# Kernel tuning notes

Hardware: AMD Instinct MI355X
Metric: run time of the kernel (lower is better)

Reference implementation:

```python
import math
import jax, jax.numpy as jnp
import numpy as np

F, B, J, D, H = 120, 64, 22, 512, 4  # frames, batch, joints, d_model, heads
DFF = 2048
EPS = 1e-6


def setup_inputs() -> dict:
    key = jax.random.key(0)
    ks = jax.random.split(key, 32)
    w = lambda k, s: jax.random.normal(k, s, jnp.float32) * 0.02
    inp = {
        "x": jax.random.normal(ks[0], (F, B, J, D), jnp.float32),
        "timesteps_embs": jax.random.normal(ks[1], (1, B, D), jnp.float32),
        "spat_mask": jnp.ones((1, 1, 1, 1, 1), jnp.int32),
        "temp_mask": jnp.ones((1, 1, 1, 1, 1), jnp.int32),
        "layer_ind": 1,
    }
    i = 2
    for p in ("s", "t"):  # spatial / temporal attention params
        for m in ("q", "k", "v", "o"):
            inp[p + "W" + m] = w(ks[i], (D, D)); i += 1
            inp[p + "b" + m] = w(ks[i], (D,)); i += 1
    inp["ffW1"] = w(ks[i], (D, DFF)); inp["ffb1"] = w(ks[i + 1], (DFF,))
    inp["ffW2"] = w(ks[i + 2], (DFF, D)); inp["ffb2"] = w(ks[i + 3], (D,))
    for n in ("n1", "n2", "n3"):
        inp[n + "a"] = jnp.ones((D,), jnp.float32)
        inp[n + "b"] = jnp.zeros((D,), jnp.float32)
    return inp


def _norm(x, a, b):
    # custom Norm: uses torch.std (ddof=1) and eps added to std (not var)
    mu = jnp.mean(x, axis=-1, keepdims=True)
    sd = jnp.std(x, axis=-1, ddof=1, keepdims=True)
    return a * (x - mu) / (sd + EPS) + b


def _mha(x, Wq, bq, Wk, bk, Wv, bv, Wo, bo, h, mask):
    d1, bs, d2, dm = x.shape
    dk = dm // h
    split = lambda t: (t.reshape(d1, bs, d2, h, dk)).transpose(0, 1, 3, 2, 4)  # (d1,bs,h,d2,dk)
    q = split(x @ Wq + bq)
    k = split(x @ Wk + bk)
    v = split(x @ Wv + bv)
    scores = jnp.einsum("fbhqd,fbhkd->fbhqk", q, k) / math.sqrt(dk)
    m = jnp.swapaxes(mask, 0, 1).astype(jnp.float32)  # mask.transpose(0,1).float()
    scores = jnp.where(m == 0, -1e9, scores)
    p = jax.nn.softmax(scores, axis=-1)
    o = jnp.einsum("fbhqk,fbhkd->fbhqd", p, v)
    o = o.transpose(0, 1, 3, 2, 4).reshape(d1, bs, d2, dm)
    return o @ Wo + bo


def _forward(x, timesteps_embs,
             sWq, sbq, sWk, sbk, sWv, sbv, sWo, sbo,
             tWq, tbq, tWk, tbk, tWv, tbv, tWo, tbo,
             ffW1, ffb1, ffW2, ffb2,
             n1a, n1b, n2a, n2b, n3a, n3b,
             spat_mask, temp_mask):
    # layer_ind > 0 path: no positional-encoding additions (eval mode: dropout = identity)
    f, bs, nj, dm = x.shape
    ts = jnp.broadcast_to(timesteps_embs[:, :, None, :], (f, bs, 1, dm))
    x1 = jnp.concatenate([ts, x], axis=2)                      # (F,B,J+1,D)
    x1 = x + _mha(x1, sWq, sbq, sWk, sbk, sWv, sbv, sWo, sbo, H, spat_mask)[:, :, 1:, :]
    x1 = jnp.swapaxes(_norm(x1, n1a, n1b), 0, 2)               # (J,B,F,D)
    ts2 = jnp.broadcast_to(timesteps_embs[:, :, None, :], (x1.shape[0], bs, 1, dm))
    x2 = jnp.concatenate([ts2, x1], axis=2)                    # (J,B,F+1,D)
    x2 = x1 + _mha(x2, tWq, tbq, tWk, tbk, tWv, tbv, tWo, tbo, H, temp_mask)[:, :, 1:, :]
    x2 = jnp.swapaxes(_norm(x2, n2a, n2b), 0, 2)               # (F,B,J,D)
    ff = jax.nn.gelu(x2 @ ffW1 + ffb1, approximate=False) @ ffW2 + ffb2
    return _norm(x2 + ff, n3a, n3b)


def reference(x, timesteps_embs,
              sWq, sbq, sWk, sbk, sWv, sbv, sWo, sbo,
              tWq, tbq, tWk, tbk, tWv, tbv, tWo, tbo,
              ffW1, ffb1, ffW2, ffb2,
              n1a, n1b, n2a, n2b, n3a, n3b,
              spat_mask, temp_mask, layer_ind):
    # layer_ind is fixed to 1 (layer_ind==0 branch is unreachable/broken in source)
    return _forward(x, timesteps_embs,
                    sWq, sbq, sWk, sbk, sWv, sbv, sWo, sbo,
                    tWq, tbq, tWk, tbk, tWv, tbv, tWo, tbo,
                    ffW1, ffb1, ffW2, ffb2,
                    n1a, n1b, n2a, n2b, n3a, n3b,
                    spat_mask, temp_mask)
```

## Files before the change

kernel.cpp:

```cpp
#include <hip/hip_runtime.h>
#include <hip/hip_bf16.h>
#include <math.h>


#define F_DIM 120
#define B_DIM 64
#define J_DIM 22
#define H_DIM 4
#define M_TOK (F_DIM * B_DIM * J_DIM)

#define DEV static __device__ __forceinline__

typedef short bf16x8 __attribute__((ext_vector_type(8)));
typedef short us8 __attribute__((ext_vector_type(8)));
typedef float f32x4 __attribute__((ext_vector_type(4)));

struct __align__(8) us4 { unsigned short x, y, z, w; };

DEV unsigned short f2b(float f) {
  unsigned u = __float_as_uint(f);
  u += 0x7fffu + ((u >> 16) & 1u);
  return (unsigned short)(u >> 16);
}
DEV float b2f(unsigned short u) { return __uint_as_float(((unsigned)u) << 16); }

#define GLOAD16(g, l)                                                          \
  __builtin_amdgcn_global_load_lds(                                            \
      (const __attribute__((address_space(1))) void*)(g),                      \
      (__attribute__((address_space(3))) void*)(l), 16, 0, 0)

enum { EPI_QKV = 0, EPI_GELU = 1, EPI_RES = 2, EPI_ACC = 3, EPI_RESB = 4,
       EPI_ROB = 5,
       EPI_RBB = 6 };

__global__ __launch_bounds__(256)
void cast_k(const float* __restrict__ in, unsigned short* __restrict__ out, int n8) {
  for (int i = blockIdx.x * 256 + threadIdx.x; i < n8; i += gridDim.x * 256) {
    const float4 a = ((const float4*)in)[i * 2];
    const float4 b = ((const float4*)in)[i * 2 + 1];
    us8 v;
    v[0] = f2b(a.x); v[1] = f2b(a.y); v[2] = f2b(a.z); v[3] = f2b(a.w);
    v[4] = f2b(b.x); v[5] = f2b(b.y); v[6] = f2b(b.z); v[7] = f2b(b.w);
    *(us8*)&out[i * 8] = v;
  }
}

__global__ __launch_bounds__(256)
void tcast_k(const float* __restrict__ W, unsigned short* __restrict__ WT, int K, int N) {
  __shared__ float t[32][33];
  const int n0 = blockIdx.x * 32, k0 = blockIdx.y * 32;
  const int tx = threadIdx.x, ty = threadIdx.y;
#pragma unroll
  for (int i = 0; i < 4; ++i)
    t[ty + i * 8][tx] = W[(size_t)(k0 + ty + i * 8) * N + n0 + tx];
  __syncthreads();
#pragma unroll
  for (int i = 0; i < 4; ++i)
    WT[(size_t)(n0 + ty + i * 8) * K + k0 + tx] = f2b(t[tx][ty + i * 8]);
}

struct Tc8Args { const float* W[8]; unsigned short* WT[8]; };
__global__ __launch_bounds__(256)
void tcast8_k(Tc8Args a) {
  __shared__ float t[32][33];
  const float* W = a.W[blockIdx.z];
  unsigned short* WT = a.WT[blockIdx.z];
  const int n0 = blockIdx.x * 32, k0 = blockIdx.y * 32;
  const int tx = threadIdx.x, ty = threadIdx.y;
#pragma unroll
  for (int i = 0; i < 4; ++i)
    t[ty + i * 8][tx] = W[(size_t)(k0 + ty + i * 8) * 512 + n0 + tx];
  __syncthreads();
#pragma unroll
  for (int i = 0; i < 4; ++i)
    WT[(size_t)(n0 + ty + i * 8) * 512 + k0 + tx] = f2b(t[tx][ty + i * 8]);
}

struct TsArgs { const float* W[4]; const float* bias[4]; unsigned short* out[4]; };
__global__ __launch_bounds__(1024)
void tsproj_k(const float* __restrict__ ts, TsArgs a) {
  __shared__ float tsr[512];
  __shared__ float red[3][256];
  const int b = blockIdx.x;
  const int nb = blockIdx.y;
  const int pj = blockIdx.z;
  const int t = threadIdx.x;
  const int n = nb * 256 + (t & 255);
  const int kh = t >> 8;
  if (t < 512) tsr[t] = ts[b * 512 + t];
  __syncthreads();
  const float* W = a.W[pj];
  float acc = 0.f;
  const int k0 = kh * 128;
  for (int k = k0; k < k0 + 128; ++k)
    acc += tsr[k] * W[(size_t)k * 512 + n];
  if (kh) red[kh - 1][t & 255] = acc;
  __syncthreads();
  if (kh == 0) {
    acc += red[0][t & 255] + red[1][t & 255] + red[2][t & 255];
    a.out[pj][b * 512 + n] = f2b(acc + a.bias[pj][n]);
  }
}

template<int EPI>
DEV void epi_store(float v, int row, int col, const float* b0, const float* b1,
                   const float* b2, const void* res, float* outF,
                   unsigned short* o0, unsigned short* o1, unsigned short* o2,
                   int ldo, float scale) {
  if constexpr (EPI == EPI_QKV) {
    const int seg = col >> 9;
    const int cl = col & 511;
    const float* bs = (seg == 0) ? b0 : (seg == 1) ? b1 : b2;
    unsigned short* ob = (seg == 0) ? o0 : (seg == 1) ? o1 : o2;
    const float sc = (seg == 0) ? scale : 1.f;
    v = (v + bs[cl]) * sc;
    ob[(size_t)row * 512 + cl] = f2b(v);
  } else if constexpr (EPI == EPI_GELU) {
    v += b0[col];
    const float a2 = 1.5957691216057308f * (v + 0.044715f * v * v * v);
    const float g = v / (1.f + __expf(-a2));
    o0[(size_t)row * ldo + col] = f2b(g);
  } else if constexpr (EPI == EPI_RES) {
    const size_t off = (size_t)row * 512 + col;
    outF[off] = v + b0[col] + ((const float*)res)[off];
  } else if constexpr (EPI == EPI_RESB) {
    const size_t off = (size_t)row * 512 + col;
    outF[off] = v + b0[col] + b2f(((const unsigned short*)res)[off]);
  } else if constexpr (EPI == EPI_ROB) {
    const size_t off = (size_t)row * 512 + col;
    o0[off] = f2b(v + b0[col] + ((const float*)res)[off]);
  } else if constexpr (EPI == EPI_RBB) {
    const size_t off = (size_t)row * 512 + col;
    o0[off] = f2b(v + b0[col] + b2f(((const unsigned short*)res)[off]));
  } else {
    const size_t off = (size_t)row * 512 + col;
    outF[off] = v + outF[off];
  }
}

template<int EPI>
__global__ __launch_bounds__(512, 4)
void gemm256_k(const unsigned short* __restrict__ Ab, const unsigned short* __restrict__ Wt,
               const float* __restrict__ b0, const float* __restrict__ b1, const float* __restrict__ b2,
               const void* __restrict__ res, float* __restrict__ outF,
               unsigned short* __restrict__ o0, unsigned short* __restrict__ o1, unsigned short* __restrict__ o2,
               int lda, int ldw, int ldo, int nk, int nx, float scale) {
  __shared__ unsigned short As[3][8192];
  __shared__ unsigned short Bs[3][4096];
  const int tid = threadIdx.x;
  const int chunkg = gridDim.x >> 3;
  const int wg = (blockIdx.x & 7) * chunkg + (blockIdx.x >> 3);
  const int nbase = (wg % nx) * 128;
  const int mbase = (wg / nx) * 256;
  const int lane = tid & 63;
  const int w = tid >> 6;
  const int wr = (w >> 1) * 64;
  const int wc = (w & 1) * 64;
  const int l15 = lane & 15;
  const int lhi = lane >> 4;

  const int crow = lane >> 2;
  const int ccol = (((lane & 3) ^ ((lane >> 3) & 3)) << 3);
  const unsigned short* gA0 = Ab + (size_t)(mbase + 32 * w + crow) * lda + ccol;
  const unsigned short* gA1 = gA0 + (size_t)16 * lda;
  const unsigned short* gB0 = Wt + (size_t)(nbase + 16 * w + crow) * ldw + ccol;

  auto stage = [&](int bb, int kt) {
    GLOAD16(gA0 + kt, &As[bb][(2 * w) * 512]);
    GLOAD16(gA1 + kt, &As[bb][(2 * w + 1) * 512]);
    GLOAD16(gB0 + kt, &Bs[bb][w * 512]);
  };

  f32x4 acc[4][4] = {};
  const int KT = nk >> 5;
  const int swz = ((lhi ^ ((l15 >> 1) & 3)) << 3);

  stage(0, 0);
  stage(1, 32);
  asm volatile("s_waitcnt vmcnt(3)" ::: "memory");
  __builtin_amdgcn_s_barrier();

  for (int t = 0; t < KT; ++t) {
    const unsigned short* as = As[t % 3];
    const unsigned short* bs = Bs[t % 3];
    if (t + 2 < KT) stage((t + 2) % 3, (t + 2) << 5);
    bf16x8 afr[4], bfr[4];
#pragma unroll
    for (int i = 0; i < 4; ++i) afr[i] = *(const bf16x8*)&as[(wr + i * 16 + l15) * 32 + swz];
#pragma unroll
    for (int j = 0; j < 4; ++j) bfr[j] = *(const bf16x8*)&bs[(wc + j * 16 + l15) * 32 + swz];
#pragma unroll
    for (int i = 0; i < 4; ++i)
#pragma unroll
      for (int j = 0; j < 4; ++j)
        acc[i][j] = __builtin_amdgcn_mfma_f32_16x16x32_bf16(afr[i], bfr[j], acc[i][j], 0, 0, 0);
    if (t + 2 < KT)      asm volatile("s_waitcnt vmcnt(3) lgkmcnt(0)" ::: "memory");
    else if (t + 1 < KT) asm volatile("s_waitcnt vmcnt(0) lgkmcnt(0)" ::: "memory");
    else                 asm volatile("s_waitcnt lgkmcnt(0)" ::: "memory");
    __builtin_amdgcn_s_barrier();
  }

#pragma unroll
  for (int i = 0; i < 4; ++i)
#pragma unroll
    for (int j = 0; j < 4; ++j) {
      const int row0 = mbase + wr + i * 16 + (lhi << 2);
      const int col = nbase + wc + j * 16 + l15;
#pragma unroll
      for (int q = 0; q < 4; ++q)
        epi_store<EPI>(acc[i][j][q], row0 + q, col, b0, b1, b2, res, outF, o0, o1, o2, ldo, scale);
    }
}

template<int EPI>
__global__ __launch_bounds__(256)
void gemm_k(const unsigned short* __restrict__ Ab, const unsigned short* __restrict__ Wt,
            const float* __restrict__ b0, const float* __restrict__ b1, const float* __restrict__ b2,
            const void* __restrict__ res, float* __restrict__ outF,
            unsigned short* __restrict__ o0, unsigned short* __restrict__ o1, unsigned short* __restrict__ o2,
            int lda, int ldw, int ldo, int nk, int nx, float scale) {
  __shared__ unsigned short As[3][4096];
  __shared__ unsigned short Bs[3][4096];
  const int tid = threadIdx.x;
  const int chunkg = gridDim.x >> 3;
  const int wg = (blockIdx.x & 7) * chunkg + (blockIdx.x >> 3);
  const int nbase = (wg % nx) * 128;
  const int mbase = (wg / nx) * 128;
  const int lane = tid & 63;
  const int w = tid >> 6;
  const int wr = (w >> 1) * 64;
  const int wc = (w & 1) * 64;
  const int l15 = lane & 15;
  const int lhi = lane >> 4;

  const int crow = lane >> 2;
  const int ccol = (((lane & 3) ^ ((lane >> 3) & 3)) << 3);
  const unsigned short* gA0 = Ab + (size_t)(mbase + 32 * w + crow) * lda + ccol;
  const unsigned short* gA1 = gA0 + (size_t)16 * lda;
  const unsigned short* gB0 = Wt + (size_t)(nbase + 32 * w + crow) * ldw + ccol;
  const unsigned short* gB1 = gB0 + (size_t)16 * ldw;

  auto stage = [&](int bb, int kt) {
    GLOAD16(gA0 + kt, &As[bb][(2 * w) * 512]);
    GLOAD16(gA1 + kt, &As[bb][(2 * w + 1) * 512]);
    GLOAD16(gB0 + kt, &Bs[bb][(2 * w) * 512]);
    GLOAD16(gB1 + kt, &Bs[bb][(2 * w + 1) * 512]);
  };

  f32x4 acc[4][4] = {};
  const int KT = nk >> 5;
  const int swz = ((lhi ^ ((l15 >> 1) & 3)) << 3);

  stage(0, 0);
  stage(1, 32);
  asm volatile("s_waitcnt vmcnt(4)" ::: "memory");
  __builtin_amdgcn_s_barrier();

  for (int t = 0; t < KT; ++t) {
    const unsigned short* as = As[t % 3];
    const unsigned short* bs = Bs[t % 3];
    if (t + 2 < KT) stage((t + 2) % 3, (t + 2) << 5);
    bf16x8 afr[4], bfr[4];
#pragma unroll
    for (int i = 0; i < 4; ++i) afr[i] = *(const bf16x8*)&as[(wr + i * 16 + l15) * 32 + swz];
#pragma unroll
    for (int j = 0; j < 4; ++j) bfr[j] = *(const bf16x8*)&bs[(wc + j * 16 + l15) * 32 + swz];
#pragma unroll
    for (int i = 0; i < 4; ++i)
#pragma unroll
      for (int j = 0; j < 4; ++j)
        acc[i][j] = __builtin_amdgcn_mfma_f32_16x16x32_bf16(afr[i], bfr[j], acc[i][j], 0, 0, 0);
    if (t + 2 < KT)      asm volatile("s_waitcnt vmcnt(4) lgkmcnt(0)" ::: "memory");
    else if (t + 1 < KT) asm volatile("s_waitcnt vmcnt(0) lgkmcnt(0)" ::: "memory");
    else                 asm volatile("s_waitcnt lgkmcnt(0)" ::: "memory");
    __builtin_amdgcn_s_barrier();
  }

#pragma unroll
  for (int i = 0; i < 4; ++i)
#pragma unroll
    for (int j = 0; j < 4; ++j) {
      const int row0 = mbase + wr + i * 16 + (lhi << 2);
      const int col = nbase + wc + j * 16 + l15;
#pragma unroll
      for (int q = 0; q < 4; ++q)
        epi_store<EPI>(acc[i][j][q], row0 + q, col, b0, b1, b2, res, outF, o0, o1, o2, ldo, scale);
    }
}

template<int EPI>
__global__ __launch_bounds__(256)
void gemmf_k(const float* __restrict__ Af, const unsigned short* __restrict__ Wt,
             const float* __restrict__ b0, const float* __restrict__ b1, const float* __restrict__ b2,
             const void* __restrict__ res, float* __restrict__ outF,
             unsigned short* __restrict__ o0, unsigned short* __restrict__ o1, unsigned short* __restrict__ o2,
             int lda, int ldw, int ldo, int nk, int nx, float scale) {
  __shared__ unsigned short As[128][40];
  __shared__ unsigned short Bs[128][40];
  const int tid = threadIdx.x;
  const int chunkg = gridDim.x >> 3;
  const int wg = (blockIdx.x & 7) * chunkg + (blockIdx.x >> 3);
  const int nbase = (wg % nx) * 128;
  const int mbase = (wg / nx) * 128;
  const int lane = tid & 63;
  const int w = tid >> 6;
  const int wr = (w >> 1) * 64;
  const int wc = (w & 1) * 64;
  const int l15 = lane & 15;
  const int lhi = lane >> 4;

  float4 ra[4];
  us4 rb[4];
  auto loadAB = [&](int kt) {
#pragma unroll
    for (int i = 0; i < 4; ++i) {
      const int g = i * 256 + tid;
      const int r = g >> 3;
      const int c = (g & 7) << 2;
      ra[i] = *(const float4*)(Af + (size_t)(mbase + r) * lda + kt + c);
      rb[i] = *(const us4*)(Wt + (size_t)(nbase + r) * ldw + kt + c);
    }
  };
  auto storeAB = [&]() {
#pragma unroll
    for (int i = 0; i < 4; ++i) {
      const int g = i * 256 + tid;
      const int r = g >> 3;
      const int c = (g & 7) << 2;
      us4 ua;
      ua.x = f2b(ra[i].x); ua.y = f2b(ra[i].y); ua.z = f2b(ra[i].z); ua.w = f2b(ra[i].w);
      *(us4*)&As[r][c] = ua;
      *(us4*)&Bs[r][c] = rb[i];
    }
  };

  f32x4 acc[4][4] = {};
  const int KT = nk >> 5;
  loadAB(0);
  storeAB();
  __syncthreads();
  for (int t = 0; t < KT; ++t) {
    if (t + 1 < KT) loadAB((t + 1) << 5);
    bf16x8 afr[4], bfr[4];
    const int klo = lhi << 3;
#pragma unroll
    for (int i = 0; i < 4; ++i) afr[i] = *(const bf16x8*)&As[wr + i * 16 + l15][klo];
#pragma unroll
    for (int j = 0; j < 4; ++j) bfr[j] = *(const bf16x8*)&Bs[wc + j * 16 + l15][klo];
#pragma unroll
    for (int i = 0; i < 4; ++i)
#pragma unroll
      for (int j = 0; j < 4; ++j)
        acc[i][j] = __builtin_amdgcn_mfma_f32_16x16x32_bf16(afr[i], bfr[j], acc[i][j], 0, 0, 0);
    __syncthreads();
    if (t + 1 < KT) { storeAB(); __syncthreads(); }
  }

#pragma unroll
  for (int i = 0; i < 4; ++i)
#pragma unroll
    for (int j = 0; j < 4; ++j) {
      const int row0 = mbase + wr + i * 16 + (lhi << 2);
      const int col = nbase + wc + j * 16 + l15;
#pragma unroll
      for (int q = 0; q < 4; ++q)
        epi_store<EPI>(acc[i][j][q], row0 + q, col, b0, b1, b2, res, outF, o0, o1, o2, ldo, scale);
    }
}

__global__ __launch_bounds__(256)
void attn_t_k(const unsigned short* __restrict__ Qb, const unsigned short* __restrict__ Kb,
              const unsigned short* __restrict__ Vb, const unsigned short* __restrict__ kts,
              const unsigned short* __restrict__ vts, unsigned short* __restrict__ Ob) {
  __shared__ unsigned short Ps[128][134];
  __shared__ unsigned short Vt[64][134];
  const int tid = threadIdx.x;
  const int inst = blockIdx.x >> 2;
  const int h = blockIdx.x & 3;
  const int b = inst & (B_DIM - 1);
  const size_t rowbase = (size_t)inst * 120;
  const int hoff = h * 128;
  const int lane = tid & 63;
  const int w = tid >> 6;
  const int wr = w * 32;
  const int l15 = lane & 15;
  const int lhi = lane >> 4;

  auto stageV = [&](int half) {
    for (int e = tid; e < 2048; e += 256) {
      const int d4 = (e & 15) << 2;
      const int key = e >> 4;
      us4 v;
      if (key <= 120) {
        const unsigned short* src = (key == 0) ? (vts + b * 512) : (Vb + (rowbase + key - 1) * 512);
        v = *(const us4*)(src + hoff + half * 64 + d4);
      } else { v.x = 0; v.y = 0; v.z = 0; v.w = 0; }
      Vt[d4 + 0][key] = v.x; Vt[d4 + 1][key] = v.y; Vt[d4 + 2][key] = v.z; Vt[d4 + 3][key] = v.w;
    }
  };
  stageV(0);

  bf16x8 qa[2][4];
#pragma unroll
  for (int i = 0; i < 2; ++i) {
    const int row = min(wr + i * 16 + l15, 119);
    const unsigned short* qp = Qb + (rowbase + row) * 512 + hoff;
#pragma unroll
    for (int kt = 0; kt < 4; ++kt)
      qa[i][kt] = *(const bf16x8*)(qp + kt * 32 + lhi * 8);
  }

  f32x4 acc[2][8] = {};
#pragma unroll
  for (int kt = 0; kt < 4; ++kt) {
    const int klo = kt * 32 + lhi * 8;
    bf16x8 kb[8];
#pragma unroll
    for (int j = 0; j < 8; ++j) {
      const int key = min(j * 16 + l15, 120);
      const unsigned short* kp = (key == 0) ? (kts + b * 512) : (Kb + (rowbase + key - 1) * 512);
      kb[j] = *(const bf16x8*)(kp + hoff + klo);
    }
#pragma unroll
    for (int i = 0; i < 2; ++i)
#pragma unroll
      for (int j = 0; j < 8; ++j)
        acc[i][j] = __builtin_amdgcn_mfma_f32_16x16x32_bf16(qa[i][kt], kb[j], acc[i][j], 0, 0, 0);
  }

  float rinv[2][4];
#pragma unroll
  for (int i = 0; i < 2; ++i)
#pragma unroll
    for (int q = 0; q < 4; ++q) {
      float m = -1e30f;
#pragma unroll
      for (int j = 0; j < 8; ++j)
        if (j * 16 + l15 <= 120) m = fmaxf(m, acc[i][j][q]);
#pragma unroll
      for (int mk = 1; mk < 16; mk <<= 1) m = fmaxf(m, __shfl_xor(m, mk, 64));
      float s = 0.f;
#pragma unroll
      for (int j = 0; j < 8; ++j) {
        const float e = (j * 16 + l15 <= 120) ? __expf(acc[i][j][q] - m) : 0.f;
        acc[i][j][q] = e; s += e;
      }
#pragma unroll
      for (int mk = 1; mk < 16; mk <<= 1) s += __shfl_xor(s, mk, 64);
      rinv[i][q] = 1.f / s;
    }

#pragma unroll
  for (int i = 0; i < 2; ++i)
#pragma unroll
    for (int j = 0; j < 8; ++j)
#pragma unroll
      for (int q = 0; q < 4; ++q)
        Ps[wr + i * 16 + lhi * 4 + q][j * 16 + l15] = f2b(acc[i][j][q]);

  __syncthreads();

#pragma unroll
  for (int half = 0; half < 2; ++half) {
    if (half == 1) {
      __syncthreads();
      stageV(1);
      __syncthreads();
    }
    f32x4 oac[2][4] = {};
#pragma unroll
    for (int kt = 0; kt < 4; ++kt) {
      const int klo = kt * 32 + lhi * 8;
      bf16x8 pa[2], vb[4];
#pragma unroll
      for (int i = 0; i < 2; ++i) pa[i] = *(const bf16x8*)&Ps[wr + i * 16 + l15][klo];
#pragma unroll
      for (int jd = 0; jd < 4; ++jd) vb[jd] = *(const bf16x8*)&Vt[jd * 16 + l15][klo];
#pragma unroll
      for (int i = 0; i < 2; ++i)
#pragma unroll
        for (int jd = 0; jd < 4; ++jd)
          oac[i][jd] = __builtin_amdgcn_mfma_f32_16x16x32_bf16(pa[i], vb[jd], oac[i][jd], 0, 0, 0);
    }
#pragma unroll
    for (int i = 0; i < 2; ++i)
#pragma unroll
      for (int q = 0; q < 4; ++q) {
        const int r = wr + i * 16 + lhi * 4 + q;
        if (r < 120) {
          const float sc = rinv[i][q];
#pragma unroll
          for (int jd = 0; jd < 4; ++jd)
            Ob[(rowbase + r) * 512 + hoff + half * 64 + jd * 16 + l15] = f2b(oac[i][jd][q] * sc);
        }
      }
  }
}

__global__ __launch_bounds__(256)
void attn_s_k(const unsigned short* __restrict__ Qb, const unsigned short* __restrict__ Kb,
              const unsigned short* __restrict__ Vb, const unsigned short* __restrict__ kts,
              const unsigned short* __restrict__ vts, unsigned short* __restrict__ Ob) {
  __shared__ unsigned short Ps[4][32][34];
  __shared__ unsigned short Vt[4][128][34];
  const int tid = threadIdx.x;
  const int inst = blockIdx.x;
  const int b = inst & (B_DIM - 1);
  const size_t rowbase = (size_t)inst * 22;
  const int lane = tid & 63;
  const int h = tid >> 6;
  const int l15 = lane & 15;
  const int lhi = lane >> 4;
  const int hoff = h * 128;

  for (int e = tid; e < 4096; e += 256) {
    const int h2 = e >> 10;
    const int rem = e & 1023;
    const int key = rem >> 5;
    const int d4 = (rem & 31) << 2;
    us4 v;
    if (key <= 22) {
      const unsigned short* src = (key == 0) ? (vts + b * 512) : (Vb + (rowbase + key - 1) * 512);
      v = *(const us4*)(src + h2 * 128 + d4);
    } else { v.x = 0; v.y = 0; v.z = 0; v.w = 0; }
    Vt[h2][d4 + 0][key] = v.x; Vt[h2][d4 + 1][key] = v.y; Vt[h2][d4 + 2][key] = v.z; Vt[h2][d4 + 3][key] = v.w;
  }

  bf16x8 qa[2][4];
#pragma unroll
  for (int i = 0; i < 2; ++i) {
    const int row = min(i * 16 + l15, 21);
    const unsigned short* qp = Qb + (rowbase + row) * 512 + hoff;
#pragma unroll
    for (int kt = 0; kt < 4; ++kt)
      qa[i][kt] = *(const bf16x8*)(qp + kt * 32 + lhi * 8);
  }

  f32x4 acc[2][2] = {};
#pragma unroll
  for (int kt = 0; kt < 4; ++kt) {
    const int klo = kt * 32 + lhi * 8;
    bf16x8 kb[2];
#pragma unroll
    for (int j = 0; j < 2; ++j) {
      const int key = min(j * 16 + l15, 22);
      const unsigned short* kp = (key == 0) ? (kts + b * 512) : (Kb + (rowbase + key - 1) * 512);
      kb[j] = *(const bf16x8*)(kp + hoff + klo);
    }
#pragma unroll
    for (int i = 0; i < 2; ++i)
#pragma unroll
      for (int j = 0; j < 2; ++j)
        acc[i][j] = __builtin_amdgcn_mfma_f32_16x16x32_bf16(qa[i][kt], kb[j], acc[i][j], 0, 0, 0);
  }

  float rinv[2][4];
#pragma unroll
  for (int i = 0; i < 2; ++i)
#pragma unroll
    for (int q = 0; q < 4; ++q) {
      float m = -1e30f;
#pragma unroll
      for (int j = 0; j < 2; ++j)
        if (j * 16 + l15 <= 22) m = fmaxf(m, acc[i][j][q]);
#pragma unroll
      for (int mk = 1; mk < 16; mk <<= 1) m = fmaxf(m, __shfl_xor(m, mk, 64));
      float s = 0.f;
#pragma unroll
      for (int j = 0; j < 2; ++j) {
        const float e = (j * 16 + l15 <= 22) ? __expf(acc[i][j][q] - m) : 0.f;
        acc[i][j][q] = e; s += e;
      }
#pragma unroll
      for (int mk = 1; mk < 16; mk <<= 1) s += __shfl_xor(s, mk, 64);
      rinv[i][q] = 1.f / s;
    }

#pragma unroll
  for (int i = 0; i < 2; ++i)
#pragma unroll
    for (int j = 0; j < 2; ++j)
#pragma unroll
      for (int q = 0; q < 4; ++q)
        Ps[h][i * 16 + lhi * 4 + q][j * 16 + l15] = f2b(acc[i][j][q]);

  __syncthreads();

  f32x4 oac[2][8] = {};
  {
    const int klo = lhi * 8;
    bf16x8 pa[2];
#pragma unroll
    for (int i = 0; i < 2; ++i) pa[i] = *(const bf16x8*)&Ps[h][i * 16 + l15][klo];
#pragma unroll
    for (int jd = 0; jd < 8; ++jd) {
      const bf16x8 vb = *(const bf16x8*)&Vt[h][jd * 16 + l15][klo];
#pragma unroll
      for (int i = 0; i < 2; ++i)
        oac[i][jd] = __builtin_amdgcn_mfma_f32_16x16x32_bf16(pa[i], vb, oac[i][jd], 0, 0, 0);
    }
  }

#pragma unroll
  for (int i = 0; i < 2; ++i)
#pragma unroll
    for (int q = 0; q < 4; ++q) {
      const int r = i * 16 + lhi * 4 + q;
      if (r < 22) {
        const float sc = rinv[i][q];
#pragma unroll
        for (int jd = 0; jd < 8; ++jd)
          Ob[(rowbase + r) * 512 + hoff + jd * 16 + l15] = f2b(oac[i][jd][q] * sc);
      }
    }
}

__global__ __launch_bounds__(256)
void norm_k(const float* __restrict__ in, float* __restrict__ out,
            unsigned short* __restrict__ outB,
            const float* __restrict__ ga, const float* __restrict__ gb, const int mode) {
  const int r = blockIdx.x * 4 + (threadIdx.x >> 6);
  const int lane = threadIdx.x & 63;
  const float* row = in + (size_t)r * 512;
  const float4 v0 = *(const float4*)&row[lane * 4];
  const float4 v1 = *(const float4*)&row[256 + lane * 4];
  float s = v0.x + v0.y + v0.z + v0.w + v1.x + v1.y + v1.z + v1.w;
  float ss = v0.x * v0.x + v0.y * v0.y + v0.z * v0.z + v0.w * v0.w
           + v1.x * v1.x + v1.y * v1.y + v1.z * v1.z + v1.w * v1.w;
#pragma unroll
  for (int m = 1; m < 64; m <<= 1) { s += __shfl_xor(s, m, 64); ss += __shfl_xor(ss, m, 64); }
  const float mean = s * (1.f / 512.f);
  const float var = (ss - 512.f * mean * mean) * (1.f / 511.f);
  const float inv = 1.f / (sqrtf(fmaxf(var, 0.f)) + 1e-6f);
  int ro;
  if (mode == 0) ro = r;
  else if (mode == 1) {
    const int f = r / (B_DIM * J_DIM);
    const int bb = (r / J_DIM) % B_DIM;
    const int j = r % J_DIM;
    ro = (j * B_DIM + bb) * F_DIM + f;
  } else {
    const int j = r / (B_DIM * F_DIM);
    const int bb = (r / F_DIM) % B_DIM;
    const int f = r % F_DIM;
    ro = (f * B_DIM + bb) * J_DIM + j;
  }
  const float4 g0 = *(const float4*)&ga[lane * 4];
  const float4 g1 = *(const float4*)&ga[256 + lane * 4];
  const float4 h0 = *(const float4*)&gb[lane * 4];
  const float4 h1 = *(const float4*)&gb[256 + lane * 4];
  float4 y0, y1;
  y0.x = g0.x * (v0.x - mean) * inv + h0.x;
  y0.y = g0.y * (v0.y - mean) * inv + h0.y;
  y0.z = g0.z * (v0.z - mean) * inv + h0.z;
  y0.w = g0.w * (v0.w - mean) * inv + h0.w;
  y1.x = g1.x * (v1.x - mean) * inv + h1.x;
  y1.y = g1.y * (v1.y - mean) * inv + h1.y;
  y1.z = g1.z * (v1.z - mean) * inv + h1.z;
  y1.w = g1.w * (v1.w - mean) * inv + h1.w;
  if (out) {
    float* orow = out + (size_t)ro * 512;
    *(float4*)&orow[lane * 4] = y0;
    *(float4*)&orow[256 + lane * 4] = y1;
  }
  if (outB) {
    us4 a, b;
    a.x = f2b(y0.x); a.y = f2b(y0.y); a.z = f2b(y0.z); a.w = f2b(y0.w);
    b.x = f2b(y1.x); b.y = f2b(y1.y); b.z = f2b(y1.z); b.w = f2b(y1.w);
    *(us4*)&outB[(size_t)ro * 512 + lane * 4] = a;
    *(us4*)&outB[(size_t)ro * 512 + 256 + lane * 4] = b;
  }
}

__global__ __launch_bounds__(256)
void normb_k(const unsigned short* __restrict__ in, float* __restrict__ out,
             unsigned short* __restrict__ outB,
             const float* __restrict__ ga, const float* __restrict__ gb, const int mode) {
  const int r = blockIdx.x * 4 + (threadIdx.x >> 6);
  const int lane = threadIdx.x & 63;
  const us8 wv = *(const us8*)&in[(size_t)r * 512 + lane * 8];
  float v[8];
  float s = 0.f, ss = 0.f;
#pragma unroll
  for (int e = 0; e < 8; ++e) {
    v[e] = b2f((unsigned short)wv[e]);
    s += v[e]; ss += v[e] * v[e];
  }
#pragma unroll
  for (int m = 1; m < 64; m <<= 1) { s += __shfl_xor(s, m, 64); ss += __shfl_xor(ss, m, 64); }
  const float mean = s * (1.f / 512.f);
  const float var = (ss - 512.f * mean * mean) * (1.f / 511.f);
  const float inv = 1.f / (sqrtf(fmaxf(var, 0.f)) + 1e-6f);
  int ro;
  if (mode == 0) ro = r;
  else if (mode == 1) {
    const int f = r / (B_DIM * J_DIM);
    const int bb = (r / J_DIM) % B_DIM;
    const int j = r % J_DIM;
    ro = (j * B_DIM + bb) * F_DIM + f;
  } else {
    const int j = r / (B_DIM * F_DIM);
    const int bb = (r / F_DIM) % B_DIM;
    const int f = r % F_DIM;
    ro = (f * B_DIM + bb) * J_DIM + j;
  }
  const float4 g0 = *(const float4*)&ga[lane * 8];
  const float4 g1 = *(const float4*)&ga[lane * 8 + 4];
  const float4 h0 = *(const float4*)&gb[lane * 8];
  const float4 h1 = *(const float4*)&gb[lane * 8 + 4];
  float y[8];
  y[0] = g0.x * (v[0] - mean) * inv + h0.x;
  y[1] = g0.y * (v[1] - mean) * inv + h0.y;
  y[2] = g0.z * (v[2] - mean) * inv + h0.z;
  y[3] = g0.w * (v[3] - mean) * inv + h0.w;
  y[4] = g1.x * (v[4] - mean) * inv + h1.x;
  y[5] = g1.y * (v[5] - mean) * inv + h1.y;
  y[6] = g1.z * (v[6] - mean) * inv + h1.z;
  y[7] = g1.w * (v[7] - mean) * inv + h1.w;
  if (out) {
    float* orow = out + (size_t)ro * 512 + lane * 8;
    *(float4*)&orow[0] = *(float4*)&y[0];
    *(float4*)&orow[4] = *(float4*)&y[4];
  }
  if (outB) {
    us8 o;
#pragma unroll
    for (int e = 0; e < 8; ++e) o[e] = f2b(y[e]);
    *(us8*)&outB[(size_t)ro * 512 + lane * 8] = o;
  }
}

extern "C" void kernel_launch(void* const* d_in, const int* in_sizes, int n_in,
                              void* d_out, int out_size, void* d_ws, size_t ws_size,
                              hipStream_t stream) {
  const float* x   = (const float*)d_in[0];
  const float* tse = (const float*)d_in[1];
  const float* sWq = (const float*)d_in[5];  const float* sbq = (const float*)d_in[6];
  const float* sWk = (const float*)d_in[7];  const float* sbk = (const float*)d_in[8];
  const float* sWv = (const float*)d_in[9];  const float* sbv = (const float*)d_in[10];
  const float* sWo = (const float*)d_in[11]; const float* sbo = (const float*)d_in[12];
  const float* tWq = (const float*)d_in[13]; const float* tbq = (const float*)d_in[14];
  const float* tWk = (const float*)d_in[15]; const float* tbk = (const float*)d_in[16];
  const float* tWv = (const float*)d_in[17]; const float* tbv = (const float*)d_in[18];
  const float* tWo = (const float*)d_in[19]; const float* tbo = (const float*)d_in[20];
  const float* ffW1 = (const float*)d_in[21]; const float* ffb1 = (const float*)d_in[22];
  const float* ffW2 = (const float*)d_in[23]; const float* ffb2 = (const float*)d_in[24];
  const float* n1a = (const float*)d_in[25]; const float* n1b = (const float*)d_in[26];
  const float* n2a = (const float*)d_in[27]; const float* n2b = (const float*)d_in[28];
  const float* n3a = (const float*)d_in[29]; const float* n3b = (const float*)d_in[30];

  char* p = (char*)d_ws;
  auto carve = [&](size_t bytes) { void* r = (void*)p; p += (bytes + 255) & ~(size_t)255; return r; };

  unsigned short* sQKVt = (unsigned short*)carve((size_t)3 * 512 * 512 * 2);
  unsigned short* sOT   = (unsigned short*)carve((size_t)512 * 512 * 2);
  unsigned short* tQKVt = (unsigned short*)carve((size_t)3 * 512 * 512 * 2);
  unsigned short* tOT   = (unsigned short*)carve((size_t)512 * 512 * 2);
  unsigned short* W1T   = (unsigned short*)carve((size_t)2048 * 512 * 2);
  unsigned short* W2T   = (unsigned short*)carve((size_t)512 * 2048 * 2);
  unsigned short* ktss  = (unsigned short*)carve((size_t)64 * 512 * 2);
  unsigned short* vtss  = (unsigned short*)carve((size_t)64 * 512 * 2);
  unsigned short* ktst  = (unsigned short*)carve((size_t)64 * 512 * 2);
  unsigned short* vtst  = (unsigned short*)carve((size_t)64 * 512 * 2);
  unsigned short* Qb    = (unsigned short*)carve((size_t)M_TOK * 512 * 2);

  unsigned short* Kb = (unsigned short*)d_out;
  unsigned short* Vb = Kb + (size_t)M_TOK * 512;
  float* outF = (float*)d_out;

  const bool bigws = ws_size >= (size_t)873725952ull;
  float* Rbuf = nullptr;
  unsigned short* Hb  = nullptr;
  unsigned short* xb  = nullptr;
  unsigned short* rb1 = nullptr;
  if (bigws) {
    Hb = (unsigned short*)carve((size_t)M_TOK * 2048 * 2);
    xb = Hb;
    rb1 = Hb + (size_t)M_TOK * 512;
  } else {
    Rbuf = (float*)carve((size_t)M_TOK * 512 * 4);
  }

  const float QSCALE = 0.08838834764831845f;

  {
    dim3 tb(32, 8);
    Tc8Args tc;
    tc.W[0] = sWq; tc.WT[0] = sQKVt;
    tc.W[1] = sWk; tc.WT[1] = sQKVt + 262144;
    tc.W[2] = sWv; tc.WT[2] = sQKVt + 524288;
    tc.W[3] = sWo; tc.WT[3] = sOT;
    tc.W[4] = tWq; tc.WT[4] = tQKVt;
    tc.W[5] = tWk; tc.WT[5] = tQKVt + 262144;
    tc.W[6] = tWv; tc.WT[6] = tQKVt + 524288;
    tc.W[7] = tWo; tc.WT[7] = tOT;
    tcast8_k<<<dim3(16, 16, 8), tb, 0, stream>>>(tc);
    tcast_k<<<dim3(64, 16), tb, 0, stream>>>(ffW1, W1T, 512, 2048);
    tcast_k<<<dim3(16, 64), tb, 0, stream>>>(ffW2, W2T, 2048, 512);
  }
  {
    TsArgs ta;
    ta.W[0] = sWk; ta.bias[0] = sbk; ta.out[0] = ktss;
    ta.W[1] = sWv; ta.bias[1] = sbv; ta.out[1] = vtss;
    ta.W[2] = tWk; ta.bias[2] = tbk; ta.out[2] = ktst;
    ta.W[3] = tWv; ta.bias[3] = tbv; ta.out[3] = vtst;
    tsproj_k<<<dim3(B_DIM, 2, 4), 1024, 0, stream>>>(tse, ta);
  }

  const int MT = M_TOK / 128;
  const int MT2 = M_TOK / 256;

  if (bigws) {
    cast_k<<<2048, 256, 0, stream>>>(x, xb, M_TOK * 512 / 8);
    gemm256_k<EPI_QKV><<<12 * MT2, 512, 0, stream>>>(
        xb, sQKVt, sbq, sbk, sbv, nullptr, nullptr, Qb, Kb, Vb, 512, 512, 512, 512, 12, QSCALE);
    attn_s_k<<<dim3(F_DIM * B_DIM), 256, 0, stream>>>(Qb, Kb, Vb, ktss, vtss, Qb);
    gemm256_k<EPI_RBB><<<4 * MT2, 512, 0, stream>>>(
        Qb, sOT, sbo, nullptr, nullptr, xb, nullptr, Kb, nullptr, nullptr, 512, 512, 512, 512, 4, 1.f);
    normb_k<<<M_TOK / 4, 256, 0, stream>>>(Kb, nullptr, rb1, n1a, n1b, 1);

    gemm256_k<EPI_QKV><<<12 * MT2, 512, 0, stream>>>(
        rb1, tQKVt, tbq, tbk, tbv, nullptr, nullptr, Qb, Kb, Vb, 512, 512, 512, 512, 12, QSCALE);
    attn_t_k<<<dim3(J_DIM * B_DIM * H_DIM), 256, 0, stream>>>(Qb, Kb, Vb, ktst, vtst, Qb);
    gemm256_k<EPI_RBB><<<4 * MT2, 512, 0, stream>>>(
        Qb, tOT, tbo, nullptr, nullptr, rb1, nullptr, Kb, nullptr, nullptr, 512, 512, 512, 512, 4, 1.f);
    normb_k<<<M_TOK / 4, 256, 0, stream>>>(Kb, nullptr, Qb, n2a, n2b, 2);

    gemm256_k<EPI_GELU><<<16 * MT2, 512, 0, stream>>>(
        Qb, W1T, ffb1, nullptr, nullptr, nullptr, nullptr, Hb, nullptr, nullptr,
        512, 512, 2048, 512, 16, 1.f);
    gemm256_k<EPI_RBB><<<4 * MT2, 512, 0, stream>>>(
        Hb, W2T, ffb2, nullptr, nullptr, Qb, nullptr, Qb, nullptr, nullptr,
        2048, 2048, 512, 2048, 4, 1.f);
    normb_k<<<M_TOK / 4, 256, 0, stream>>>(Qb, outF, nullptr, n3a, n3b, 0);
  } else {
    gemmf_k<EPI_QKV><<<12 * MT, 256, 0, stream>>>(
        x, sQKVt, sbq, sbk, sbv, nullptr, nullptr, Qb, Kb, Vb, 512, 512, 512, 512, 12, QSCALE);
    attn_s_k<<<dim3(F_DIM * B_DIM), 256, 0, stream>>>(Qb, Kb, Vb, ktss, vtss, Qb);
    gemm_k<EPI_RES><<<4 * MT, 256, 0, stream>>>(
        Qb, sOT, sbo, nullptr, nullptr, x, outF, nullptr, nullptr, nullptr, 512, 512, 512, 512, 4, 1.f);
    norm_k<<<M_TOK / 4, 256, 0, stream>>>(outF, Rbuf, nullptr, n1a, n1b, 1);

    gemmf_k<EPI_QKV><<<12 * MT, 256, 0, stream>>>(
        Rbuf, tQKVt, tbq, tbk, tbv, nullptr, nullptr, Qb, Kb, Vb, 512, 512, 512, 512, 12, QSCALE);
    attn_t_k<<<dim3(J_DIM * B_DIM * H_DIM), 256, 0, stream>>>(Qb, Kb, Vb, ktst, vtst, Qb);
    gemm_k<EPI_RES><<<4 * MT, 256, 0, stream>>>(
        Qb, tOT, tbo, nullptr, nullptr, Rbuf, outF, nullptr, nullptr, nullptr, 512, 512, 512, 512, 4, 1.f);
    norm_k<<<M_TOK / 4, 256, 0, stream>>>(outF, Rbuf, Qb, n2a, n2b, 2);

    for (int c = 0; c < 4; ++c) {
      gemm_k<EPI_GELU><<<4 * MT, 256, 0, stream>>>(
          Qb, W1T + (size_t)c * 512 * 512, ffb1 + c * 512, nullptr, nullptr,
          nullptr, nullptr, Qb, nullptr, nullptr, 512, 512, 512, 512, 4, 1.f);
      if (c == 0)
        gemm_k<EPI_RES><<<4 * MT, 256, 0, stream>>>(
            Qb, W2T + c * 512, ffb2, nullptr, nullptr, Rbuf, outF,
            nullptr, nullptr, nullptr, 512, 2048, 512, 512, 4, 1.f);
      else
        gemm_k<EPI_ACC><<<4 * MT, 256, 0, stream>>>(
            Qb, W2T + c * 512, nullptr, nullptr, nullptr, nullptr, outF,
            nullptr, nullptr, nullptr, 512, 2048, 512, 512, 4, 1.f);
    }
    norm_k<<<M_TOK / 4, 256, 0, stream>>>(outF, outF, nullptr, n3a, n3b, 0);
  }
}
```

Before: 3.085 ms.

## Stage bf16 GEMM epilogue through swizzled LDS for coalesced 16-byte stores

For the QKV, GELU and residual-bf16 epilogues, the GEMM now writes bias-added (and activated) results into a swizzled LDS tile, one 128-row half at a time. It then reads them back as 8-element vectors and issues coalesced nontemporal global stores, fusing the bf16 residual add into that pass. This replaces scattered 2-byte stores straight from MFMA accumulator layout. Separately, the cast and norm kernels switch their stores to nontemporal hints. The cost is extra LDS traffic and two barriers per half, and nontemporal stores may hurt if a later kernel would have hit the outputs in cache.

```diff
diff --git a/kernel.cpp b/kernel.cpp
--- a/kernel.cpp
+++ b/kernel.cpp
@@ -30,8 +30,7 @@
       (__attribute__((address_space(3))) void*)(l), 16, 0, 0)
 
 enum { EPI_QKV = 0, EPI_GELU = 1, EPI_RES = 2, EPI_ACC = 3, EPI_RESB = 4,
-       EPI_ROB = 5,
-       EPI_RBB = 6 };
+       EPI_ROB = 5, EPI_RBB = 6 };
 
 __global__ __launch_bounds__(256)
 void cast_k(const float* __restrict__ in, unsigned short* __restrict__ out, int n8) {
@@ -41,7 +40,7 @@
     us8 v;
     v[0] = f2b(a.x); v[1] = f2b(a.y); v[2] = f2b(a.z); v[3] = f2b(a.w);
     v[4] = f2b(b.x); v[5] = f2b(b.y); v[6] = f2b(b.z); v[7] = f2b(b.w);
-    *(us8*)&out[i * 8] = v;
+    __builtin_nontemporal_store(v, (us8*)&out[i * 8]);
   }
 }
 
@@ -200,16 +199,71 @@
     __builtin_amdgcn_s_barrier();
   }
 
-#pragma unroll
-  for (int i = 0; i < 4; ++i)
-#pragma unroll
-    for (int j = 0; j < 4; ++j) {
-      const int row0 = mbase + wr + i * 16 + (lhi << 2);
-      const int col = nbase + wc + j * 16 + l15;
-#pragma unroll
-      for (int q = 0; q < 4; ++q)
-        epi_store<EPI>(acc[i][j][q], row0 + q, col, b0, b1, b2, res, outF, o0, o1, o2, ldo, scale);
-    }
+  if constexpr (EPI == EPI_QKV || EPI == EPI_GELU || EPI == EPI_RBB) {
+    unsigned short* Ot = &As[0][0];
+    const int seg = (EPI == EPI_QKV) ? (nbase >> 9) : 0;
+    unsigned short* ob = (EPI == EPI_QKV) ? ((seg == 0) ? o0 : (seg == 1) ? o1 : o2) : o0;
+    const float* bb = (EPI == EPI_QKV) ? ((seg == 0) ? b0 : (seg == 1) ? b1 : b2) : b0;
+    const float sc = (EPI == EPI_QKV && 0 == seg) ? scale : 1.f;
+    const int cb = (EPI == EPI_QKV) ? (nbase & 511) : nbase;
+#pragma unroll
+    for (int mh = 0; mh < 2; ++mh) {
+      if ((w >> 2) == mh) {
+        const int lwr = ((w >> 1) & 1) * 64;
+#pragma unroll
+        for (int i = 0; i < 4; ++i)
+#pragma unroll
+          for (int j = 0; j < 4; ++j) {
+            const int c = wc + j * 16 + l15;
+#pragma unroll
+            for (int q = 0; q < 4; ++q) {
+              const int lrow = lwr + i * 16 + (lhi << 2) + q;
+              float v = acc[i][j][q];
+              if constexpr (EPI == EPI_QKV) {
+                v = (v + bb[cb + c]) * sc;
+              } else if constexpr (EPI == EPI_GELU) {
+                v += bb[cb + c];
+                const float a2 = 1.5957691216057308f * (v + 0.044715f * v * v * v);
+                v = v / (1.f + __expf(-a2));
+              } else {
+                v += bb[cb + c];
+              }
+              Ot[(lrow << 7) + ((((c >> 3) ^ (lrow & 7)) << 3) | (c & 7))] = f2b(v);
+            }
+          }
+      }
+      __syncthreads();
+#pragma unroll
+      for (int ps = 0; ps < 4; ++ps) {
+        const int idx = (ps * 512 + tid) * 8;
+        const int row = idx >> 7;
+        const int c = idx & 127;
+        us8 val = *(const us8*)&Ot[(row << 7) + (((c >> 3) ^ (row & 7)) << 3)];
+        const size_t grow = (size_t)(mbase + mh * 128 + row);
+        const int gcol = cb + c;
+        if constexpr (EPI == EPI_RBB) {
+          const us8 r = __builtin_nontemporal_load(
+              (const us8*)&((const unsigned short*)res)[grow * 512 + gcol]);
+#pragma unroll
+          for (int e = 0; e < 8; ++e)
+            val[e] = (short)f2b(b2f((unsigned short)val[e]) + b2f((unsigned short)r[e]));
+        }
+        __builtin_nontemporal_store(val, (us8*)&ob[grow * ldo + gcol]);
+      }
+      __syncthreads();
+    }
+  } else {
+#pragma unroll
+    for (int i = 0; i < 4; ++i)
+#pragma unroll
+      for (int j = 0; j < 4; ++j) {
+        const int row0 = mbase + wr + i * 16 + (lhi << 2);
+        const int col = nbase + wc + j * 16 + l15;
+#pragma unroll
+        for (int q = 0; q < 4; ++q)
+          epi_store<EPI>(acc[i][j][q], row0 + q, col, b0, b1, b2, res, outF, o0, o1, o2, ldo, scale);
+      }
+  }
 }
 
 template<int EPI>
@@ -719,14 +773,14 @@
   y[7] = g1.w * (v[7] - mean) * inv + h1.w;
   if (out) {
     float* orow = out + (size_t)ro * 512 + lane * 8;
-    *(float4*)&orow[0] = *(float4*)&y[0];
-    *(float4*)&orow[4] = *(float4*)&y[4];
+    __builtin_nontemporal_store(*(f32x4*)&y[0], (f32x4*)&orow[0]);
+    __builtin_nontemporal_store(*(f32x4*)&y[4], (f32x4*)&orow[4]);
   }
   if (outB) {
     us8 o;
 #pragma unroll
     for (int e = 0; e < 8; ++e) o[e] = f2b(y[e]);
-    *(us8*)&outB[(size_t)ro * 512 + lane * 8] = o;
+    __builtin_nontemporal_store(o, (us8*)&outB[(size_t)ro * 512 + lane * 8]);
   }
 }
 
```

Measured after the change: 2.982 ms. -3.3%, faster.
